# Kernel tuning notes

Hardware: AMD Instinct MI355X
Metric: run time of the kernel (lower is better)

The kernel has to match this reference:

```python
import math
import jax, jax.numpy as jnp
import numpy as np

N_HEAD = 16
N_EMBD = 2048
HEAD_DIM = N_EMBD // N_HEAD  # 128
ROPE_BASE = 10000.0
EPS = 1e-12  # F.normalize eps


def setup_inputs() -> dict:
    key = jax.random.key(0)
    ks = jax.random.split(key, 5)
    B, T, C = 2, 2048, N_EMBD
    s = 0.02
    return {
        "x": jax.random.normal(ks[0], (B, T, C), jnp.float32),
        "Wq": jax.random.normal(ks[1], (C, C), jnp.float32) * s,
        "Wk": jax.random.normal(ks[2], (C, C), jnp.float32) * s,
        "Wv": jax.random.normal(ks[3], (C, C), jnp.float32) * s,
        "Wo": jax.random.normal(ks[4], (C, C), jnp.float32) * s,
        "qk_scale": jnp.ones((HEAD_DIM,), jnp.float32) / math.sqrt(N_EMBD),
    }


def _rope(x, cos, sin):
    # x: [B,T,H,D], cos/sin: [T, D/2] broadcast as [1,T,1,D/2]
    d = x.shape[-1] // 2
    x1, x2 = x[..., :d], x[..., d:]
    c = cos[None, :, None, :]
    s = sin[None, :, None, :]
    return jnp.concatenate([x1 * c + x2 * s, -x1 * s + x2 * c], axis=-1)


def reference(x, Wq, Wk, Wv, Wo, qk_scale):
    B, T, C = x.shape
    H, D = N_HEAD, HEAD_DIM

    q = (x @ Wq.T).reshape(B, T, H, D)
    k = (x @ Wk.T).reshape(B, T, H, D)
    v = (x @ Wv.T).reshape(B, T, H, D)

    # L2-normalize over head_dim, then per-channel scale (scaler() = param * sqrt(n_embd))
    scale_vec = qk_scale * math.sqrt(N_EMBD)  # == 1.0 at init
    q = scale_vec * (q / jnp.maximum(jnp.linalg.norm(q, axis=-1, keepdims=True), EPS))
    k = scale_vec * (k / jnp.maximum(jnp.linalg.norm(k, axis=-1, keepdims=True), EPS))

    # rotary embeddings (half-split, non-interleaved)
    inv_freq = 1.0 / (ROPE_BASE ** (jnp.arange(0, D, 2, dtype=jnp.float32) / D))
    freqs = jnp.arange(T, dtype=jnp.float32)[:, None] * inv_freq[None, :]  # [T, D/2]
    cos, sin = jnp.cos(freqs), jnp.sin(freqs)
    q = _rope(q, cos, sin)
    k = _rope(k, cos, sin)

    # causal SDPA with scale = sqrt(head_dim) (as in the source)
    scores = jnp.einsum("bthd,bshd->bhts", q, k) * math.sqrt(D)  # [B,H,T,T]
    causal = jnp.tril(jnp.ones((T, T), bool))
    scores = jnp.where(causal[None, None], scores, -jnp.inf)
    attn = jax.nn.softmax(scores, axis=-1)
    y = jnp.einsum("bhts,bshd->bthd", attn, v).reshape(B, T, C)
    return y @ Wo.T
```

## Files before the change

### kernel.cpp

```cpp
#include <hip/hip_runtime.h>
#include <math.h>

typedef _Float16 f16;
typedef _Float16 f16x2 __attribute__((ext_vector_type(2)));
typedef _Float16 f16x4 __attribute__((ext_vector_type(4)));
typedef _Float16 f16x8 __attribute__((ext_vector_type(8)));
typedef __fp16 fp16x2 __attribute__((ext_vector_type(2)));
typedef float f32x4 __attribute__((ext_vector_type(4)));
typedef float f32x16 __attribute__((ext_vector_type(16)));
typedef unsigned int u32;

#define T_ 2048
#define H_ 16
#define C_ 2048

__device__ __forceinline__ void gload_lds16(const f16* g, f16* l) {
  __builtin_amdgcn_global_load_lds((const __attribute__((address_space(1))) u32*)g,
                                   (__attribute__((address_space(3))) u32*)l, 16, 0, 0);
}

__device__ __forceinline__ u32 pkk(float x, float y) {
  union { fp16x2 h; u32 u; } z;
  z.h = __builtin_amdgcn_cvt_pkrtz(x, y);
  return z.u;
}

__global__ __launch_bounds__(256) void cast_all_kernel(
    const float* __restrict__ x, const float* __restrict__ wq, const float* __restrict__ wk,
    const float* __restrict__ wv, const float* __restrict__ wo,
    f16* __restrict__ xh, f16* __restrict__ wqh, f16* __restrict__ wkh,
    f16* __restrict__ wvh, f16* __restrict__ woh) {
  int b = blockIdx.x;
  const float* src; f16* dst; size_t off;
  if (b < 8192) { src = x; dst = xh; off = (size_t)b * 1024; }
  else {
    int s = (b - 8192) >> 12, bb = (b - 8192) & 4095;
    off = (size_t)bb * 1024;
    if (s == 0) { src = wq; dst = wqh; }
    else if (s == 1) { src = wk; dst = wkh; }
    else if (s == 2) { src = wv; dst = wvh; }
    else { src = wo; dst = woh; }
  }
  size_t i = off + (size_t)threadIdx.x * 4;
  float4 v = *(const float4*)&src[i];
  f16x4 o; o[0] = (f16)v.x; o[1] = (f16)v.y; o[2] = (f16)v.z; o[3] = (f16)v.w;
  *(f16x4*)&dst[i] = o;
}

template<typename OutT>
__device__ __forceinline__ void gemm128(const f16* __restrict__ A, const f16* __restrict__ Bm,
                                        OutT* __restrict__ Cm, f16* As, f16* Bs,
                                        int brow, int bcol) {
  const int K = 2048, N = 2048;
  const int tid = threadIdx.x, l = tid & 63, w = tid >> 6;
  const int lr = l & 15, lg = l >> 4;
  const int wr = (w >> 1) * 64, wc = (w & 1) * 64;
  const int srow = l >> 2, scol = (l & 3) * 8;
  const f16* gA0 = A + (size_t)(brow + w * 32 + srow) * K + scol;
  const f16* gA1 = gA0 + (size_t)16 * K;
  const f16* gB0 = Bm + (size_t)(bcol + w * 32 + srow) * K + scol;
  const f16* gB1 = gB0 + (size_t)16 * K;
  f16* lA0 = &As[(w * 32 + 0) * 32];
  f16* lA1 = &As[(w * 32 + 16) * 32];
  f16* lB0 = &Bs[(w * 32 + 0) * 32];
  f16* lB1 = &Bs[(w * 32 + 16) * 32];
  f32x4 acc[4][4] = {};
  for (int kt = 0; kt < K; kt += 32) {
    gload_lds16(gA0 + kt, lA0);
    gload_lds16(gA1 + kt, lA1);
    gload_lds16(gB0 + kt, lB0);
    gload_lds16(gB1 + kt, lB1);
    __syncthreads();
    f16x8 af[4], bf[4];
#pragma unroll
    for (int m = 0; m < 4; ++m) af[m] = *(const f16x8*)&As[(wr + m * 16 + lr) * 32 + lg * 8];
#pragma unroll
    for (int n = 0; n < 4; ++n) bf[n] = *(const f16x8*)&Bs[(wc + n * 16 + lr) * 32 + lg * 8];
#pragma unroll
    for (int m = 0; m < 4; ++m)
#pragma unroll
      for (int n = 0; n < 4; ++n)
        acc[m][n] = __builtin_amdgcn_mfma_f32_16x16x32_f16(af[m], bf[n], acc[m][n], 0, 0, 0);
    __syncthreads();
  }
#pragma unroll
  for (int m = 0; m < 4; ++m) {
    int row0 = brow + wr + m * 16 + lg * 4;
#pragma unroll
    for (int n = 0; n < 4; ++n) {
      int col = bcol + wc + n * 16 + lr;
#pragma unroll
      for (int j = 0; j < 4; ++j)
        Cm[(size_t)(row0 + j) * N + col] = (OutT)acc[m][n][j];
    }
  }
}

__global__ __launch_bounds__(256) void gemm_qkv_kernel(
    const f16* __restrict__ A, const f16* __restrict__ Wq, const f16* __restrict__ Wk,
    const f16* __restrict__ Wv, f16* __restrict__ Qo, f16* __restrict__ Ko, f16* __restrict__ Vo) {
  __shared__ f16 As[4096], Bs[4096];
  const f16* Bm; f16* Cm;
  if (blockIdx.z == 0) { Bm = Wq; Cm = Qo; }
  else if (blockIdx.z == 1) { Bm = Wk; Cm = Ko; }
  else { Bm = Wv; Cm = Vo; }
  int lin = blockIdx.y * 32 + blockIdx.x;
  int swz = (lin & 7) * 64 + (lin >> 3);
  gemm128<f16>(A, Bm, Cm, As, Bs, (swz & 31) * 128, (swz >> 5) * 128);
}

__global__ __launch_bounds__(256) void gemm_out_kernel(
    const f16* __restrict__ A, const f16* __restrict__ Wo, float* __restrict__ Cm) {
  __shared__ f16 As[4096], Bs[4096];
  int lin = blockIdx.y * 32 + blockIdx.x;
  int swz = (lin & 7) * 64 + (lin >> 3);
  gemm128<float>(A, Wo, Cm, As, Bs, (swz & 31) * 128, (swz >> 5) * 128);
}

__global__ __launch_bounds__(256) void normrope_kernel(f16* __restrict__ qp, f16* __restrict__ kp,
                                                       const float* __restrict__ qk_scale) {
  int w = threadIdx.x >> 6, l = threadIdx.x & 63;
  f16* q = blockIdx.y == 0 ? qp : kp;
  float fac = blockIdx.y == 0 ? 512.0f : 45.254833995939045f;
  int row = blockIdx.x * 4 + w;
  int t = (row >> 4) & (T_ - 1);
  size_t base = (size_t)row * 128;
  float x1 = (float)q[base + l], x2 = (float)q[base + 64 + l];
  float ss = x1 * x1 + x2 * x2;
#pragma unroll
  for (int m = 1; m < 64; m <<= 1) ss += __shfl_xor(ss, m);
  float inv = 1.0f / fmaxf(sqrtf(ss), 1e-12f);
  float sc1 = qk_scale[l] * fac;
  float sc2 = qk_scale[l + 64] * fac;
  float s1 = x1 * inv * sc1, s2 = x2 * inv * sc2;
  float invf = exp2f(-(float)l * 0.20762050593046013f);
  float ang = (float)t * invf;
  float sn, cs; sincosf(ang, &sn, &cs);
  q[base + l] = (f16)(s1 * cs + s2 * sn);
  q[base + 64 + l] = (f16)(-s1 * sn + s2 * cs);
}

#define VSTR 36
__global__ __launch_bounds__(256, 2) void attn_kernel(
    const f16* __restrict__ Q, const f16* __restrict__ K, const f16* __restrict__ V,
    f16* __restrict__ Y, f16* __restrict__ Op, float* __restrict__ ml) {
  __shared__ f16 Ks[2][32 * 128];
  __shared__ f16 Vt[2][128 * VSTR];
  const int tid = threadIdx.x, l = tid & 63, w = tid >> 6;
  const int lq = l & 31, hi = l >> 5;
  const int bid = blockIdx.x;
  const int swzb = (bid & 7) * 160 + (bid >> 3);
  const int bh = swzb / 40;
  const int cidx = swzb - bh * 40;
  int qi, j;
  if (cidx < 4)       { qi = cidx;                  j = 0; }
  else if (cidx < 12) { qi = 4 + ((cidx - 4) >> 1); j = (cidx - 4) & 1; }
  else if (cidx < 24) { qi = 8 + (cidx - 12) / 3;   j = (cidx - 12) % 3; }
  else                { qi = 12 + ((cidx - 24) >> 2); j = (cidx - 24) & 3; }
  const int nch = (qi >> 2) + 1;
  const bool multi = nch > 1;
  const int qb = qi * 128;
  const int s0kv = j * 512;
  const int endkv = min(s0kv + 512, qb + 128);
  const int nt = (endkv - s0kv) >> 5;
  const int tbase = s0kv >> 5;
  const int lastit = qi * 4 + w;
  int cid = 0;
  if (multi) {
    int pre = (qi < 8) ? (qi - 4) * 2 : (qi < 12 ? 8 + (qi - 8) * 3 : 20 + (qi - 12) * 4);
    cid = bh * 36 + pre + j;
  }
  const int b = bh >> 4, h = bh & 15;
  const size_t hb = ((size_t)b * T_ * H_ + h) * 128;
  const int qw = qb + w * 32;
  const int q = qw + lq;

  f16x8 qB[8];
  {
    const f16* qp = Q + hb + (size_t)q * 2048 + hi * 8;
#pragma unroll
    for (int dc = 0; dc < 8; ++dc) qB[dc] = *(const f16x8*)(qp + dc * 16);
  }

  const int vpr = tid & 15;
  const int vdg = (tid >> 4) * 8;
  f16x8 vr0a, vr1a;

  auto stageK = [&](int kv0, int buf) {
#pragma unroll
    for (int i = 0; i < 2; ++i) {
      int rbase = w * 8 + i * 4;
      int row_in = rbase + (l >> 4);
      const f16* kg = K + hb + (size_t)(kv0 + row_in) * 2048 + (((l & 15) ^ (row_in & 15)) << 3);
      gload_lds16(kg, &Ks[buf][rbase * 128]);
    }
  };
  auto loadV = [&](int kv0) {
    const f16* vsrc = V + hb + (size_t)(kv0 + 2 * vpr) * 2048 + vdg;
    vr0a = *(const f16x8*)(vsrc);
    vr1a = *(const f16x8*)(vsrc + 2048);
  };
  auto writeV = [&](int buf) {
#pragma unroll
    for (int jj = 0; jj < 8; ++jj) {
      union { f16x2 h2; u32 u; } p0;
      p0.h2[0] = vr0a[jj]; p0.h2[1] = vr1a[jj];
      *(u32*)&Vt[buf][(vdg + jj) * VSTR + 2 * vpr] = p0.u;
    }
  };

  stageK(s0kv, 0);
  loadV(s0kv);
  asm volatile("s_waitcnt vmcnt(0)" ::: "memory");
  writeV(0);
  __syncthreads();

  float mreg = -INFINITY, rsum = 0.f;
  f32x16 o0 = {}, o1 = {}, o2 = {}, o3 = {};

  for (int it = 0; it < nt; ++it) {
    const int cur = it & 1;
    const int kv0 = s0kv + it * 32;
    const bool havenext = (it + 1 < nt);
    if (havenext) { stageK(kv0 + 32, cur ^ 1); loadV(kv0 + 32); }

    const int ti = tbase + it;
    if (ti <= lastit) {
      const char* kB = (const char*)&Ks[cur][0];
      const int rowoff = lq * 256, kmask = (lq & 15) * 16;
      f32x16 s0 = {};
      __builtin_amdgcn_s_setprio(1);
#pragma unroll
      for (int dc = 0; dc < 8; ++dc) {
        f16x8 kf = *(const f16x8*)(kB + rowoff + ((dc * 32 + hi * 16) ^ kmask));
        s0 = __builtin_amdgcn_mfma_f32_32x32x16_f16(kf, qB[dc], s0, 0, 0, 0);
      }
      __builtin_amdgcn_s_setprio(0);
      if (ti == lastit) {
#pragma unroll
        for (int r = 0; r < 16; ++r) {
          int crow = (r & 3) + 8 * (r >> 2) + 4 * hi;
          s0[r] = (kv0 + crow <= q) ? s0[r] : -INFINITY;
        }
      }
      float t8[8];
#pragma unroll
      for (int r = 0; r < 8; ++r) t8[r] = fmaxf(s0[r], s0[r + 8]);
#pragma unroll
      for (int off = 4; off > 0; off >>= 1)
#pragma unroll
        for (int r = 0; r < off; ++r) t8[r] = fmaxf(t8[r], t8[r + off]);
      float pm = fmaxf(t8[0], __shfl_xor(t8[0], 32));
      if (multi) {
        float mn = fmaxf(mreg, pm);
        float al = __expf(mreg - mn);
        o0 *= al; o1 *= al; o2 *= al; o3 *= al;
        rsum *= al; mreg = mn;
      } else if (__any(pm > mreg + 8.0f)) {
        float mn = fmaxf(mreg, pm);
        float al = __expf(mreg - mn);
        o0 *= al; o1 *= al; o2 *= al; o3 *= al;
        rsum *= al; mreg = mn;
      }
      float sum = 0.f;
#pragma unroll
      for (int r = 0; r < 16; ++r) { float e = __expf(s0[r] - mreg); s0[r] = e; sum += e; }
      sum += __shfl_xor(sum, 32);
      rsum += sum;
      __builtin_amdgcn_s_setprio(1);
#define PVSTEP(SV, BB, KS)                                                          \
      {                                                                             \
        u32 a0 = pkk(SV[8*BB+0], SV[8*BB+1]);                                       \
        u32 a1 = pkk(SV[8*BB+2], SV[8*BB+3]);                                       \
        u32 b0 = pkk(SV[8*BB+4], SV[8*BB+5]);                                       \
        u32 b1 = pkk(SV[8*BB+6], SV[8*BB+7]);                                       \
        u32 r0 = __shfl_xor(hi ? a0 : b0, 32);                                      \
        u32 r1 = __shfl_xor(hi ? a1 : b1, 32);                                      \
        union { u32 u[4]; f16x8 v; } pf;                                            \
        pf.u[0] = hi ? r0 : a0; pf.u[1] = hi ? r1 : a1;                             \
        pf.u[2] = hi ? b0 : r0; pf.u[3] = hi ? b1 : r1;                             \
        const f16* vb = &Vt[cur][lq * VSTR + (KS) * 16 + hi * 8];                   \
        o0 = __builtin_amdgcn_mfma_f32_32x32x16_f16(*(const f16x8*)(vb), pf.v, o0, 0, 0, 0); \
        o1 = __builtin_amdgcn_mfma_f32_32x32x16_f16(*(const f16x8*)(vb + 32 * VSTR), pf.v, o1, 0, 0, 0); \
        o2 = __builtin_amdgcn_mfma_f32_32x32x16_f16(*(const f16x8*)(vb + 64 * VSTR), pf.v, o2, 0, 0, 0); \
        o3 = __builtin_amdgcn_mfma_f32_32x32x16_f16(*(const f16x8*)(vb + 96 * VSTR), pf.v, o3, 0, 0, 0); \
      }
      PVSTEP(s0, 0, 0)
      PVSTEP(s0, 1, 1)
#undef PVSTEP
      __builtin_amdgcn_s_setprio(0);
    }
    if (havenext) {
      asm volatile("s_waitcnt vmcnt(0)" ::: "memory");
      writeV(cur ^ 1);
      __syncthreads();
    }
  }

  if (!multi) {
    float inv = 1.0f / rsum;
    const size_t yb = ((size_t)(b * T_ + q)) * 2048 + h * 128;
#define OSTORE(OV, DT)                                                   \
    {                                                                    \
      _Pragma("unroll")                                                  \
      for (int g = 0; g < 4; ++g) {                                      \
        f16x4 pk;                                                        \
        pk[0] = (f16)(OV[g * 4 + 0] * inv); pk[1] = (f16)(OV[g * 4 + 1] * inv); \
        pk[2] = (f16)(OV[g * 4 + 2] * inv); pk[3] = (f16)(OV[g * 4 + 3] * inv); \
        *(f16x4*)&Y[yb + (DT) * 32 + g * 8 + 4 * hi] = pk;               \
      }                                                                  \
    }
    OSTORE(o0, 0) OSTORE(o1, 1) OSTORE(o2, 2) OSTORE(o3, 3)
#undef OSTORE
  } else {
    const size_t ob = (size_t)cid * 16384 + (size_t)(w * 32 + lq) * 128;
#define OSTORE(OV, DT)                                                   \
    {                                                                    \
      _Pragma("unroll")                                                  \
      for (int g = 0; g < 4; ++g) {                                      \
        f16x4 pk;                                                        \
        pk[0] = (f16)OV[g * 4 + 0]; pk[1] = (f16)OV[g * 4 + 1];          \
        pk[2] = (f16)OV[g * 4 + 2]; pk[3] = (f16)OV[g * 4 + 3];          \
        *(f16x4*)&Op[ob + (DT) * 32 + g * 8 + 4 * hi] = pk;              \
      }                                                                  \
    }
    OSTORE(o0, 0) OSTORE(o1, 1) OSTORE(o2, 2) OSTORE(o3, 3)
#undef OSTORE
    if (hi == 0) {
      ml[(size_t)cid * 256 + (w * 32 + lq) * 2] = mreg;
      ml[(size_t)cid * 256 + (w * 32 + lq) * 2 + 1] = rsum;
    }
  }
}

__global__ __launch_bounds__(256) void merge_kernel(const f16* __restrict__ Op,
                                                    const float* __restrict__ ml,
                                                    f16* __restrict__ Y) {
  const int g = blockIdx.x;
  const int bh = g / 12, qi = 4 + (g - 12 * (g / 12));
  const int b = bh >> 4, h = bh & 15;
  const int nch = (qi >> 2) + 1;
  const int pre = (qi < 8) ? (qi - 4) * 2 : (qi < 12 ? 8 + (qi - 8) * 3 : 20 + (qi - 12) * 4);
  const int cid0 = bh * 36 + pre;
  const int row = threadIdx.x >> 1;
  const int dh = (threadIdx.x & 1) * 64;
  float mc[4], lc[4], wgt[4];
  float M = -INFINITY;
#pragma unroll
  for (int c = 0; c < 4; ++c)
    if (c < nch) {
      mc[c] = ml[(size_t)(cid0 + c) * 256 + row * 2];
      lc[c] = ml[(size_t)(cid0 + c) * 256 + row * 2 + 1];
      M = fmaxf(M, mc[c]);
    }
  float lsum = 0.f;
#pragma unroll
  for (int c = 0; c < 4; ++c)
    if (c < nch) { wgt[c] = __expf(mc[c] - M); lsum += lc[c] * wgt[c]; }
  float inv = 1.0f / lsum;
#pragma unroll
  for (int c = 0; c < 4; ++c)
    if (c < nch) wgt[c] *= inv;
  const int t = qi * 128 + row;
  const size_t yb = ((size_t)(b * T_ + t)) * 2048 + h * 128 + dh;
  const size_t rb = (size_t)row * 128 + dh;
#pragma unroll
  for (int dblk = 0; dblk < 64; dblk += 8) {
    float acc[8] = {};
#pragma unroll
    for (int c = 0; c < 4; ++c)
      if (c < nch) {
        f16x8 v = *(const f16x8*)&Op[(size_t)(cid0 + c) * 16384 + rb + dblk];
#pragma unroll
        for (int k = 0; k < 8; ++k) acc[k] += wgt[c] * (float)v[k];
      }
    f16x8 o;
#pragma unroll
    for (int k = 0; k < 8; ++k) o[k] = (f16)acc[k];
    *(f16x8*)&Y[yb + dblk] = o;
  }
}

extern "C" void kernel_launch(void* const* d_in, const int* in_sizes, int n_in,
                              void* d_out, int out_size, void* d_ws, size_t ws_size,
                              hipStream_t stream) {
  const float* x  = (const float*)d_in[0];
  const float* Wq = (const float*)d_in[1];
  const float* Wk = (const float*)d_in[2];
  const float* Wv = (const float*)d_in[3];
  const float* Wo = (const float*)d_in[4];
  const float* qk_scale = (const float*)d_in[5];
  float* out = (float*)d_out;
  char* ws = (char*)d_ws;

  f16* xh  = (f16*)(ws);
  f16* wqh = (f16*)(ws + 16777216);
  f16* wkh = (f16*)(ws + 25165824);
  f16* wvh = (f16*)(ws + 33554432);
  f16* woh = (f16*)(ws + 41943040);
  f16* qh  = (f16*)(ws + 50331648);
  f16* kh  = (f16*)(ws + 67108864);
  f16* vh  = (f16*)(ws + 83886080);
  f16* yh  = (f16*)(ws + 100663296);
  f16*   Op  = (f16*)(ws);
  float* mlp = (float*)(ws + 37748736);

  cast_all_kernel<<<dim3(24576), dim3(256), 0, stream>>>(x, Wq, Wk, Wv, Wo, xh, wqh, wkh, wvh, woh);
  gemm_qkv_kernel<<<dim3(32, 16, 3), dim3(256), 0, stream>>>(xh, wqh, wkh, wvh, qh, kh, vh);
  normrope_kernel<<<dim3(16384, 2), dim3(256), 0, stream>>>(qh, kh, qk_scale);
  attn_kernel<<<dim3(1280), dim3(256), 0, stream>>>(qh, kh, vh, yh, Op, mlp);
  merge_kernel<<<dim3(384), dim3(256), 0, stream>>>(Op, mlp, yh);
  gemm_out_kernel<<<dim3(32, 16), dim3(256), 0, stream>>>(yh, woh, out);
}
```

Before: 381.6 us.

## Triple-buffer K/V staging in attention with two-deep prefetch

Converts the attention loop's K/V LDS staging from double to triple buffering so loads for tile it+2 are in flight while tile it is computed. Partial vmcnt waits let the barrier proceed without draining the newest prefetch. V registers alternate between two sets, and launch bounds go from 2 to 3 blocks per SM. The multi-chunk rescale now runs only when the row max increases. The cost is more LDS and register pressure, and the hand-counted vmcnt(4) must match the number of outstanding loads for the ordering to stay correct.

```diff
diff --git a/kernel.cpp b/kernel.cpp
--- a/kernel.cpp
+++ b/kernel.cpp
@@ -141,11 +141,11 @@
 }
 
 #define VSTR 36
-__global__ __launch_bounds__(256, 2) void attn_kernel(
+__global__ __launch_bounds__(256, 3) void attn_kernel(
     const f16* __restrict__ Q, const f16* __restrict__ K, const f16* __restrict__ V,
     f16* __restrict__ Y, f16* __restrict__ Op, float* __restrict__ ml) {
-  __shared__ f16 Ks[2][32 * 128];
-  __shared__ f16 Vt[2][128 * VSTR];
+  __shared__ f16 Ks[3][32 * 128];
+  __shared__ f16 Vt[3][128 * VSTR];
   const int tid = threadIdx.x, l = tid & 63, w = tid >> 6;
   const int lq = l & 31, hi = l >> 5;
   const int bid = blockIdx.x;
@@ -184,7 +184,7 @@
 
   const int vpr = tid & 15;
   const int vdg = (tid >> 4) * 8;
-  f16x8 vr0a, vr1a;
+  f16x8 vA0, vA1, vB0, vB1;
 
   auto stageK = [&](int kv0, int buf) {
 #pragma unroll
@@ -195,34 +195,51 @@
       gload_lds16(kg, &Ks[buf][rbase * 128]);
     }
   };
-  auto loadV = [&](int kv0) {
+  auto loadVA = [&](int kv0) {
     const f16* vsrc = V + hb + (size_t)(kv0 + 2 * vpr) * 2048 + vdg;
-    vr0a = *(const f16x8*)(vsrc);
-    vr1a = *(const f16x8*)(vsrc + 2048);
+    vA0 = *(const f16x8*)(vsrc);
+    vA1 = *(const f16x8*)(vsrc + 2048);
   };
-  auto writeV = [&](int buf) {
+  auto loadVB = [&](int kv0) {
+    const f16* vsrc = V + hb + (size_t)(kv0 + 2 * vpr) * 2048 + vdg;
+    vB0 = *(const f16x8*)(vsrc);
+    vB1 = *(const f16x8*)(vsrc + 2048);
+  };
+  auto writeVA = [&](int buf) {
 #pragma unroll
     for (int jj = 0; jj < 8; ++jj) {
       union { f16x2 h2; u32 u; } p0;
-      p0.h2[0] = vr0a[jj]; p0.h2[1] = vr1a[jj];
+      p0.h2[0] = vA0[jj]; p0.h2[1] = vA1[jj];
       *(u32*)&Vt[buf][(vdg + jj) * VSTR + 2 * vpr] = p0.u;
     }
   };
-
-  stageK(s0kv, 0);
-  loadV(s0kv);
+  auto writeVB = [&](int buf) {
+#pragma unroll
+    for (int jj = 0; jj < 8; ++jj) {
+      union { f16x2 h2; u32 u; } p0;
+      p0.h2[0] = vB0[jj]; p0.h2[1] = vB1[jj];
+      *(u32*)&Vt[buf][(vdg + jj) * VSTR + 2 * vpr] = p0.u;
+    }
+  };
+
+  stageK(s0kv, 0); loadVA(s0kv);
+  stageK(s0kv + 32, 1); loadVB(s0kv + 32);
   asm volatile("s_waitcnt vmcnt(0)" ::: "memory");
-  writeV(0);
-  __syncthreads();
+  writeVA(0);
+  asm volatile("s_waitcnt lgkmcnt(0)" ::: "memory");
+  __builtin_amdgcn_s_barrier();
+  asm volatile("" ::: "memory");
 
   float mreg = -INFINITY, rsum = 0.f;
   f32x16 o0 = {}, o1 = {}, o2 = {}, o3 = {};
 
   for (int it = 0; it < nt; ++it) {
-    const int cur = it & 1;
+    const int cur = it % 3;
     const int kv0 = s0kv + it * 32;
-    const bool havenext = (it + 1 < nt);
-    if (havenext) { stageK(kv0 + 32, cur ^ 1); loadV(kv0 + 32); }
+    if (it + 2 < nt) {
+      stageK(kv0 + 64, (it + 2) % 3);
+      if ((it & 1) == 0) loadVA(kv0 + 64); else loadVB(kv0 + 64);
+    }
 
     const int ti = tbase + it;
     if (ti <= lastit) {
@@ -252,10 +269,11 @@
         for (int r = 0; r < off; ++r) t8[r] = fmaxf(t8[r], t8[r + off]);
       float pm = fmaxf(t8[0], __shfl_xor(t8[0], 32));
       if (multi) {
-        float mn = fmaxf(mreg, pm);
-        float al = __expf(mreg - mn);
-        o0 *= al; o1 *= al; o2 *= al; o3 *= al;
-        rsum *= al; mreg = mn;
+        if (pm > mreg) {
+          float al = __expf(mreg - pm);
+          o0 *= al; o1 *= al; o2 *= al; o3 *= al;
+          rsum *= al; mreg = pm;
+        }
       } else if (__any(pm > mreg + 8.0f)) {
         float mn = fmaxf(mreg, pm);
         float al = __expf(mreg - mn);
@@ -290,10 +308,14 @@
 #undef PVSTEP
       __builtin_amdgcn_s_setprio(0);
     }
-    if (havenext) {
-      asm volatile("s_waitcnt vmcnt(0)" ::: "memory");
-      writeV(cur ^ 1);
-      __syncthreads();
+
+    if (it + 1 < nt) {
+      if (it + 2 < nt) asm volatile("s_waitcnt vmcnt(4)" ::: "memory");
+      else             asm volatile("s_waitcnt vmcnt(0)" ::: "memory");
+      if ((it & 1) == 0) writeVB((it + 1) % 3); else writeVA((it + 1) % 3);
+      asm volatile("s_waitcnt lgkmcnt(0)" ::: "memory");
+      __builtin_amdgcn_s_barrier();
+      asm volatile("" ::: "memory");
     }
   }
 
```

Result: slower. 558.1 us (+46.3%).
